# Kernel optimization log

Hardware: AMD Instinct MI355X
Metric: run time of the kernel (lower is better)

## Reference

```python
import jax, jax.numpy as jnp
import numpy as np

B, S, H, T = 32, 512, 1024, 32


def setup_inputs() -> dict:
    key = jax.random.key(0)
    ks = jax.random.split(key, 8)
    hidden = jax.random.normal(ks[0], (B, S, H), dtype=jnp.float32)
    W = jax.random.normal(ks[1], (H, T), dtype=jnp.float32) * 0.02
    b = jax.random.normal(ks[2], (T,), dtype=jnp.float32) * 0.02
    start_trans = jax.random.normal(ks[3], (T,), dtype=jnp.float32) * 0.1
    end_trans = jax.random.normal(ks[4], (T,), dtype=jnp.float32) * 0.1
    trans = jax.random.normal(ks[5], (T, T), dtype=jnp.float32) * 0.1
    tags = jax.random.randint(ks[6], (B, S), 0, T, dtype=jnp.int64)
    # variable-length mask: first position always valid (CRF requirement)
    lengths = jax.random.randint(ks[7], (B,), S // 2, S + 1)
    mask = jnp.arange(S)[None, :] < lengths[:, None]  # [B,S] bool
    return {"hidden": hidden, "W": W, "b": b, "start_trans": start_trans,
            "end_trans": end_trans, "trans": trans, "tags": tags, "mask": mask}


def reference(hidden, W, b, start_trans, end_trans, trans, tags, mask):
    # emission = log_softmax(fc(last_hidden_state))  [B,S,T]
    emissions = jax.nn.log_softmax(jnp.einsum('bsh,ht->bst', hidden, W) + b, axis=-1)
    maskf = mask.astype(emissions.dtype)

    # --- numerator: score of the gold tag path ---
    emit_tag = jnp.take_along_axis(emissions, tags[..., None], axis=-1)[..., 0]  # [B,S]
    trans_tag = trans[tags[:, :-1], tags[:, 1:]]                                  # [B,S-1]
    num = (start_trans[tags[:, 0]]
           + (emit_tag * maskf).sum(axis=1)
           + (trans_tag * maskf[:, 1:]).sum(axis=1))
    seq_len = mask.sum(axis=1).astype(jnp.int32)                                  # [B]
    last_tags = jnp.take_along_axis(tags, (seq_len - 1)[:, None].astype(tags.dtype), axis=1)[:, 0]
    num = num + end_trans[last_tags]

    # --- denominator: forward algorithm (masked logsumexp recurrence) ---
    alpha0 = start_trans[None, :] + emissions[:, 0]  # [B,T]

    def step(alpha, inp):
        em_t, m_t = inp  # [B,T], [B]
        nxt = jax.nn.logsumexp(alpha[:, :, None] + trans[None] + em_t[:, None, :], axis=1)
        return jnp.where(m_t[:, None], nxt, alpha), None

    em_rest = jnp.moveaxis(emissions[:, 1:], 1, 0)  # [S-1,B,T]
    m_rest = jnp.moveaxis(mask[:, 1:], 1, 0)        # [S-1,B]
    alpha, _ = jax.lax.scan(step, alpha0, (em_rest, m_rest))
    denom = jax.nn.logsumexp(alpha + end_trans[None], axis=1)  # [B]

    llh = num - denom        # CRF returns per-batch log-likelihood
    return -llh.mean()       # loss = (-crf(...)).mean()
```

## Files before the change

### kernel.cpp

```cpp
#include <hip/hip_runtime.h>
#include <hip/hip_bf16.h>


#define Bb 32
#define Ss 512
#define Hh 1024
#define Tt 32
#define NROWS (Bb*Ss)
#define NCHUNK 32
#define CHUNK_L 16

typedef __attribute__((ext_vector_type(8))) short bf16x8;
typedef __attribute__((ext_vector_type(4))) float f32x4;

__device__ __forceinline__ short f2bf(float f) {
  union { float f; unsigned u; } v; v.f = f;
  unsigned u = v.u;
  return (short)((u + 0x7FFFu + ((u >> 16) & 1u)) >> 16);
}

__global__ __launch_bounds__(128) void wpack_kernel(
    const float* __restrict__ W, short* __restrict__ Wpk,
    float* __restrict__ out) {
  const int k = blockIdx.x * 128 + threadIdx.x;
  if (k == 0) out[0] = 0.f;
#pragma unroll
  for (int t = 0; t < 32; ++t)
    Wpk[t * Hh + k] = f2bf(W[k * 32 + t]);
}

__global__ __launch_bounds__(256) void emis_fused_kernel(
    const float* __restrict__ hidden, const short* __restrict__ Wpk,
    const float* __restrict__ bias, float* __restrict__ logem) {
  __shared__ __align__(16) char smem[32768];
  float* red = (float*)smem;
  const int tid = threadIdx.x;
  const int wv = tid >> 6, lane = tid & 63;
  const int n = lane & 15, q = lane >> 4;
  const int row0 = blockIdx.x * 16;
  const int koff = wv * 256;

  {
    const int swv = tid >> 6;
    const int skc = (tid >> 3) & 7;
    const int sq = (tid >> 1) & 3;
    const int sj0 = (tid & 1) * 4;
    const int rbase = swv * 8192 + skc * 1024 + sj0 * 2;
    const int uxor = skc * 32;
    const float* hp = hidden + (size_t)row0 * Hh + 4 * tid;
#pragma unroll
    for (int i = 0; i < 16; ++i) {
      const float4 v = *(const float4*)(hp + (size_t)i * Hh);
      uint2 u;
      u.x = (unsigned short)f2bf(v.x) | ((unsigned)(unsigned short)f2bf(v.y) << 16);
      u.y = (unsigned short)f2bf(v.z) | ((unsigned)(unsigned short)f2bf(v.w) << 16);
      const int unit = ((i * 4 + sq) * 16) ^ uxor;
      *(uint2*)(smem + rbase + unit) = u;
    }
  }
  __syncthreads();

  const short* bpl = Wpk + n * Hh + koff;
  const short* bpr = Wpk + (16 + n) * Hh + koff;
  f32x4 d0 = {0.f, 0.f, 0.f, 0.f}, d1 = {0.f, 0.f, 0.f, 0.f};
#pragma unroll
  for (int kc = 0; kc < 8; ++kc) {
    const int aaddr = wv * 8192 + kc * 1024 + (((n * 4 + q) * 16) ^ (kc * 32));
    const bf16x8 a = *(const bf16x8*)(smem + aaddr);
    const bf16x8 wl = *(const bf16x8*)(bpl + kc * 32 + 8 * q);
    const bf16x8 wr = *(const bf16x8*)(bpr + kc * 32 + 8 * q);
    d0 = __builtin_amdgcn_mfma_f32_16x16x32_bf16(a, wl, d0, 0, 0, 0);
    d1 = __builtin_amdgcn_mfma_f32_16x16x32_bf16(a, wr, d1, 0, 0, 0);
  }
  __syncthreads();

#pragma unroll
  for (int r = 0; r < 4; ++r) {
    red[(wv * 16 + 4 * q + r) * 33 + n] = d0[r];
    red[(wv * 16 + 4 * q + r) * 33 + 16 + n] = d1[r];
  }
  __syncthreads();

  const int row = tid >> 4, c0 = tid & 15, c1 = 16 + c0;
  float v0 = 0.f, v1 = 0.f;
#pragma unroll
  for (int w = 0; w < 4; ++w) {
    v0 += red[(w * 16 + row) * 33 + c0];
    v1 += red[(w * 16 + row) * 33 + c1];
  }
  const float L0 = v0 + bias[c0], L1 = v1 + bias[c1];
  float mx = fmaxf(L0, L1);
#pragma unroll
  for (int d = 8; d >= 1; d >>= 1) mx = fmaxf(mx, __shfl_xor(mx, d, 16));
  float se = __expf(L0 - mx) + __expf(L1 - mx);
#pragma unroll
  for (int d = 8; d >= 1; d >>= 1) se += __shfl_xor(se, d, 16);
  const float corr = mx + __logf(se);
  const size_t rb = (size_t)(row0 + row) * Tt;
  logem[rb + c0] = L0 - corr;
  logem[rb + c1] = L1 - corr;
}

__global__ __launch_bounds__(256) void chunk_kernel(
    const float* __restrict__ logem, const float* __restrict__ trans,
    const int* __restrict__ mask, float* __restrict__ ecT,
    float* __restrict__ moff, float* __restrict__ cmax) {
  __shared__ __align__(16) float Pbuf[4 * 32 * 36];
  const int tid = threadIdx.x;
  const int wv = tid >> 6, lane = tid & 63;
  const int n = lane & 15, q = lane >> 4;
  const int chunk = blockIdx.x * 4 + wv;
  const int b = chunk >> 5, cc = chunk & 31;
  float* P = Pbuf + wv * 32 * 36;

  float etr0[8], etr1[8];
#pragma unroll
  for (int jj = 0; jj < 8; ++jj) {
    etr0[jj] = __expf(trans[(8 * q + jj) * 32 + n]);
    etr1[jj] = __expf(trans[(8 * q + jj) * 32 + 16 + n]);
  }

  const int t0 = 1 + cc * CHUNK_L;
  const int rowbase = b * Ss + t0;
  int pred = 0;
  if (lane < 16 && t0 + lane < Ss) pred = mask[rowbase + lane];
  const unsigned long long bal = __ballot(pred != 0);
  const int nst = __popcll(bal & 0xFFFFull);

  bf16x8 a0, a1;
#pragma unroll
  for (int jj = 0; jj < 8; ++jj) {
    a0[jj] = (n == 8 * q + jj) ? (short)0x3F80 : (short)0;
    a1[jj] = (16 + n == 8 * q + jj) ? (short)0x3F80 : (short)0;
  }

  f32x4 d00, d01, d10, d11;
  if (nst == 0) {
#pragma unroll
    for (int r = 0; r < 4; ++r) {
      d00[r] = (4 * q + r == n) ? 1.f : 0.f;
      d01[r] = 0.f;
      d10[r] = 0.f;
      d11[r] = (4 * q + r == n) ? 1.f : 0.f;
    }
  }
  float em0 = 0.f, em1 = 0.f;
  if (nst > 0) {
    em0 = __expf(logem[(size_t)rowbase * Tt + n]);
    em1 = __expf(logem[(size_t)rowbase * Tt + 16 + n]);
  }
  for (int st = 0; st < nst; ++st) {
    float em0n = 0.f, em1n = 0.f;
    if (st + 1 < nst) {
      em0n = __expf(logem[(size_t)(rowbase + st + 1) * Tt + n]);
      em1n = __expf(logem[(size_t)(rowbase + st + 1) * Tt + 16 + n]);
    }
    bf16x8 bL, bR;
#pragma unroll
    for (int jj = 0; jj < 8; ++jj) {
      bL[jj] = f2bf(etr0[jj] * em0);
      bR[jj] = f2bf(etr1[jj] * em1);
    }
    const f32x4 z = {0.f, 0.f, 0.f, 0.f};
    d00 = __builtin_amdgcn_mfma_f32_16x16x32_bf16(a0, bL, z, 0, 0, 0);
    d01 = __builtin_amdgcn_mfma_f32_16x16x32_bf16(a0, bR, z, 0, 0, 0);
    d10 = __builtin_amdgcn_mfma_f32_16x16x32_bf16(a1, bL, z, 0, 0, 0);
    d11 = __builtin_amdgcn_mfma_f32_16x16x32_bf16(a1, bR, z, 0, 0, 0);
    if (st + 1 < nst) {
#pragma unroll
      for (int r = 0; r < 4; ++r) {
        P[(4 * q + r) * 36 + n] = d00[r];
        P[(4 * q + r) * 36 + 16 + n] = d01[r];
        P[(16 + 4 * q + r) * 36 + n] = d10[r];
        P[(16 + 4 * q + r) * 36 + 16 + n] = d11[r];
      }
      asm volatile("s_waitcnt lgkmcnt(0)" ::: "memory");
      __builtin_amdgcn_sched_barrier(0);
      const float4 lo0 = *(const float4*)&P[n * 36 + 8 * q];
      const float4 lo1 = *(const float4*)&P[n * 36 + 8 * q + 4];
      const float4 hi0 = *(const float4*)&P[(16 + n) * 36 + 8 * q];
      const float4 hi1 = *(const float4*)&P[(16 + n) * 36 + 8 * q + 4];
      a0[0] = f2bf(lo0.x); a0[1] = f2bf(lo0.y); a0[2] = f2bf(lo0.z); a0[3] = f2bf(lo0.w);
      a0[4] = f2bf(lo1.x); a0[5] = f2bf(lo1.y); a0[6] = f2bf(lo1.z); a0[7] = f2bf(lo1.w);
      a1[0] = f2bf(hi0.x); a1[1] = f2bf(hi0.y); a1[2] = f2bf(hi0.z); a1[3] = f2bf(hi0.w);
      a1[4] = f2bf(hi1.x); a1[5] = f2bf(hi1.y); a1[6] = f2bf(hi1.z); a1[7] = f2bf(hi1.w);
    }
    em0 = em0n; em1 = em1n;
  }

  float lg0[4], lg1[4], iv0[4], iv1[4];
#pragma unroll
  for (int r = 0; r < 4; ++r) {
    float m0v = fmaxf(d00[r], d01[r]);
    float m1v = fmaxf(d10[r], d11[r]);
#pragma unroll
    for (int d = 8; d >= 1; d >>= 1) {
      m0v = fmaxf(m0v, __shfl_xor(m0v, d, 16));
      m1v = fmaxf(m1v, __shfl_xor(m1v, d, 16));
    }
    m0v = fmaxf(m0v, 1e-37f);
    m1v = fmaxf(m1v, 1e-37f);
    lg0[r] = __logf(m0v); iv0[r] = __builtin_amdgcn_rcpf(m0v);
    lg1[r] = __logf(m1v); iv1[r] = __builtin_amdgcn_rcpf(m1v);
  }
  float* E = ecT + (size_t)(b * NCHUNK + cc) * 32 * 32;
  {
    float4 s;
    s = make_float4(d00[0] * iv0[0], d00[1] * iv0[1], d00[2] * iv0[2], d00[3] * iv0[3]);
    *(float4*)&E[n * 32 + 4 * q] = s;
    s = make_float4(d10[0] * iv1[0], d10[1] * iv1[1], d10[2] * iv1[2], d10[3] * iv1[3]);
    *(float4*)&E[n * 32 + 16 + 4 * q] = s;
    s = make_float4(d01[0] * iv0[0], d01[1] * iv0[1], d01[2] * iv0[2], d01[3] * iv0[3]);
    *(float4*)&E[(16 + n) * 32 + 4 * q] = s;
    s = make_float4(d11[0] * iv1[0], d11[1] * iv1[1], d11[2] * iv1[2], d11[3] * iv1[3]);
    *(float4*)&E[(16 + n) * 32 + 16 + 4 * q] = s;
  }
  if (n == 0) {
    float* Mo = moff + (size_t)(b * NCHUNK + cc) * 32;
    *(float4*)&Mo[4 * q] = make_float4(lg0[0], lg0[1], lg0[2], lg0[3]);
    *(float4*)&Mo[16 + 4 * q] = make_float4(lg1[0], lg1[1], lg1[2], lg1[3]);
  }
  {
    float cm = fmaxf(fmaxf(fmaxf(lg0[0], lg0[1]), fmaxf(lg0[2], lg0[3])),
                     fmaxf(fmaxf(lg1[0], lg1[1]), fmaxf(lg1[2], lg1[3])));
    cm = fmaxf(cm, __shfl_xor(cm, 16));
    cm = fmaxf(cm, __shfl_xor(cm, 32));
    if (lane == 0) cmax[b * NCHUNK + cc] = cm;
  }
}

__global__ __launch_bounds__(64) void phase2_kernel(
    const float* __restrict__ logem, const float* __restrict__ start_trans,
    const float* __restrict__ end_trans, const float* __restrict__ ecT,
    const float* __restrict__ moff, const float* __restrict__ cmax,
    const float* __restrict__ trans, const int* __restrict__ tags,
    const int* __restrict__ mask, float* __restrict__ out) {
  const int b = blockIdx.x;
  const int lane = threadIdx.x;
  const int j = lane & 31;
  __shared__ __align__(16) float qlds[32];

  const int base_row = b * Ss;
  int lensum = 0;
  float snum = 0.f;
#pragma unroll
  for (int k = 0; k < 8; ++k) {
    const int ss = lane + 64 * k;
    const int m = mask[base_row + ss];
    lensum += m;
    if (m) {
      const int tg = tags[base_row + ss];
      snum += logem[(size_t)(base_row + ss) * Tt + tg];
      if (ss > 0) snum += trans[tags[base_row + ss - 1] * Tt + tg];
    }
  }
#pragma unroll
  for (int d = 32; d >= 1; d >>= 1) {
    snum += __shfl_xor(snum, d);
    lensum += __shfl_xor(lensum, d);
  }

  const float* base = ecT + (size_t)b * NCHUNK * 32 * 32;
  const float* mbase = moff + (size_t)b * NCHUNK * 32;
  const float cm_l = cmax[b * NCHUNK + j];

  float4 M[8], N[8];
  const float* r0 = base + j * 32;
#pragma unroll
  for (int k = 0; k < 8; ++k) M[k] = *(const float4*)(r0 + 4 * k);
  float mo_cur = mbase[j];

  float al0 = start_trans[j] + logem[(size_t)base_row * Tt + j];
  float m0 = al0;
#pragma unroll
  for (int d = 16; d >= 1; d >>= 1) m0 = fmaxf(m0, __shfl_xor(m0, d, 32));
  float a = __expf(al0 - m0);
  float Mb = m0;
  const float eend = __expf(end_trans[j]);

  float mo_next = 0.f;
  for (int c = 0; c < NCHUNK; ++c) {
    if (c + 1 < NCHUNK) {
      const float* rn = base + ((c + 1) * 32 + j) * 32;
#pragma unroll
      for (int k = 0; k < 8; ++k) N[k] = *(const float4*)(rn + 4 * k);
      mo_next = mbase[(c + 1) * 32 + j];
    }
    const float mom = __shfl(cm_l, c, 32);
    const float qv = a * __expf(mo_cur - mom);
    if (lane < 32) qlds[j] = qv;
    asm volatile("s_waitcnt lgkmcnt(0)" ::: "memory");
    __builtin_amdgcn_sched_barrier(0);
    float s0 = 0.f, s1 = 0.f, s2 = 0.f, s3 = 0.f;
#pragma unroll
    for (int k = 0; k < 8; ++k) {
      const float4 q4 = *(const float4*)(qlds + 4 * k);
      float* sp = (k & 1) ? ((k & 2) ? &s3 : &s1) : ((k & 2) ? &s2 : &s0);
      *sp = fmaf(q4.x, M[k].x, *sp);
      *sp = fmaf(q4.y, M[k].y, *sp);
      *sp = fmaf(q4.z, M[k].z, *sp);
      *sp = fmaf(q4.w, M[k].w, *sp);
    }
    const float s = (s0 + s1) + (s2 + s3);
    Mb += mom;
    if ((c & 3) == 3) {
      float m = s;
#pragma unroll
      for (int d = 16; d >= 1; d >>= 1) m = fmaxf(m, __shfl_xor(m, d, 32));
      m = fmaxf(m, 1e-30f);
      a = s * __builtin_amdgcn_rcpf(m);
      Mb += __logf(m);
    } else {
      a = s;
    }
#pragma unroll
    for (int k = 0; k < 8; ++k) M[k] = N[k];
    mo_cur = mo_next;
  }
  float z = a * eend;
#pragma unroll
  for (int d = 16; d >= 1; d >>= 1) z += __shfl_xor(z, d, 32);
  if (lane == 0) {
    const float numfull = snum + start_trans[tags[base_row]] +
                          end_trans[tags[base_row + lensum - 1]];
    const float denom = Mb + __logf(z);
    atomicAdd(out, -(numfull - denom) * (1.0f / 32.0f));
  }
}

extern "C" void kernel_launch(void* const* d_in, const int* in_sizes, int n_in,
                              void* d_out, int out_size, void* d_ws, size_t ws_size,
                              hipStream_t stream) {
  const float* hidden = (const float*)d_in[0];
  const float* W = (const float*)d_in[1];
  const float* bias = (const float*)d_in[2];
  const float* start_trans = (const float*)d_in[3];
  const float* end_trans = (const float*)d_in[4];
  const float* trans = (const float*)d_in[5];
  const int* tags = (const int*)d_in[6];
  const int* mask = (const int*)d_in[7];
  float* out = (float*)d_out;

  float* logem = (float*)d_ws;
  float* ecT = logem + (size_t)NROWS * Tt;
  float* moff = ecT + (size_t)Bb * NCHUNK * 32 * 32;
  float* cmax = moff + (size_t)Bb * NCHUNK * 32;
  short* Wpk = (short*)(cmax + (size_t)Bb * NCHUNK);

  wpack_kernel<<<8, 128, 0, stream>>>(W, Wpk, out);
  emis_fused_kernel<<<NROWS / 16, 256, 0, stream>>>(hidden, Wpk, bias, logem);
  chunk_kernel<<<Bb * NCHUNK / 4, 256, 0, stream>>>(logem, trans, mask, ecT, moff, cmax);
  phase2_kernel<<<Bb, 64, 0, stream>>>(logem, start_trans, end_trans, ecT, moff,
                                       cmax, trans, tags, mask, out);
}
```

Before: 151.1 us.

## Fuse chunk and phase2 kernels into one per-batch kernel with interleaved chunks

Merges the chunk-matrix kernel and the sequential phase2 kernel into a single per-batch block of 8 waves. Each wave processes two chunks interleaved per pass to hide MFMA and LDS latency. moff and cmax stay in shared memory, and the LDS ping-pong buffer is stored as bf16 so it reloads directly as MFMA operands. The emission factor is now applied after the MFMA instead of folded into the B operand. This removes one launch and some global traffic, but only 32 blocks run the chunk work, where the previous chunk kernel spread it over 256 blocks.

```diff
diff --git a/kernel.cpp b/kernel.cpp
--- a/kernel.cpp
+++ b/kernel.cpp
@@ -41,11 +41,10 @@
   const int koff = wv * 256;
 
   {
-    const int swv = tid >> 6;
     const int skc = (tid >> 3) & 7;
     const int sq = (tid >> 1) & 3;
     const int sj0 = (tid & 1) * 4;
-    const int rbase = swv * 8192 + skc * 1024 + sj0 * 2;
+    const int rbase = (tid >> 6) * 8192 + skc * 1024 + sj0 * 2;
     const int uxor = skc * 32;
     const float* hp = hidden + (size_t)row0 * Hh + 4 * tid;
 #pragma unroll
@@ -101,40 +100,10 @@
   logem[rb + c1] = L1 - corr;
 }
 
-__global__ __launch_bounds__(256) void chunk_kernel(
-    const float* __restrict__ logem, const float* __restrict__ trans,
-    const int* __restrict__ mask, float* __restrict__ ecT,
-    float* __restrict__ moff, float* __restrict__ cmax) {
-  __shared__ __align__(16) float Pbuf[4 * 32 * 36];
-  const int tid = threadIdx.x;
-  const int wv = tid >> 6, lane = tid & 63;
-  const int n = lane & 15, q = lane >> 4;
-  const int chunk = blockIdx.x * 4 + wv;
-  const int b = chunk >> 5, cc = chunk & 31;
-  float* P = Pbuf + wv * 32 * 36;
-
-  float etr0[8], etr1[8];
-#pragma unroll
-  for (int jj = 0; jj < 8; ++jj) {
-    etr0[jj] = __expf(trans[(8 * q + jj) * 32 + n]);
-    etr1[jj] = __expf(trans[(8 * q + jj) * 32 + 16 + n]);
-  }
-
-  const int t0 = 1 + cc * CHUNK_L;
-  const int rowbase = b * Ss + t0;
-  int pred = 0;
-  if (lane < 16 && t0 + lane < Ss) pred = mask[rowbase + lane];
-  const unsigned long long bal = __ballot(pred != 0);
-  const int nst = __popcll(bal & 0xFFFFull);
-
-  bf16x8 a0, a1;
-#pragma unroll
-  for (int jj = 0; jj < 8; ++jj) {
-    a0[jj] = (n == 8 * q + jj) ? (short)0x3F80 : (short)0;
-    a1[jj] = (16 + n == 8 * q + jj) ? (short)0x3F80 : (short)0;
-  }
-
-  f32x4 d00, d01, d10, d11;
+__device__ __forceinline__ void chunk_epilogue(
+    f32x4 d00, f32x4 d01, f32x4 d10, f32x4 d11, int nst,
+    int n, int q, int lane, float* __restrict__ E,
+    float* __restrict__ moff_row, float* __restrict__ cmaxp) {
   if (nst == 0) {
 #pragma unroll
     for (int r = 0; r < 4; ++r) {
@@ -144,50 +113,6 @@
       d11[r] = (4 * q + r == n) ? 1.f : 0.f;
     }
   }
-  float em0 = 0.f, em1 = 0.f;
-  if (nst > 0) {
-    em0 = __expf(logem[(size_t)rowbase * Tt + n]);
-    em1 = __expf(logem[(size_t)rowbase * Tt + 16 + n]);
-  }
-  for (int st = 0; st < nst; ++st) {
-    float em0n = 0.f, em1n = 0.f;
-    if (st + 1 < nst) {
-      em0n = __expf(logem[(size_t)(rowbase + st + 1) * Tt + n]);
-      em1n = __expf(logem[(size_t)(rowbase + st + 1) * Tt + 16 + n]);
-    }
-    bf16x8 bL, bR;
-#pragma unroll
-    for (int jj = 0; jj < 8; ++jj) {
-      bL[jj] = f2bf(etr0[jj] * em0);
-      bR[jj] = f2bf(etr1[jj] * em1);
-    }
-    const f32x4 z = {0.f, 0.f, 0.f, 0.f};
-    d00 = __builtin_amdgcn_mfma_f32_16x16x32_bf16(a0, bL, z, 0, 0, 0);
-    d01 = __builtin_amdgcn_mfma_f32_16x16x32_bf16(a0, bR, z, 0, 0, 0);
-    d10 = __builtin_amdgcn_mfma_f32_16x16x32_bf16(a1, bL, z, 0, 0, 0);
-    d11 = __builtin_amdgcn_mfma_f32_16x16x32_bf16(a1, bR, z, 0, 0, 0);
-    if (st + 1 < nst) {
-#pragma unroll
-      for (int r = 0; r < 4; ++r) {
-        P[(4 * q + r) * 36 + n] = d00[r];
-        P[(4 * q + r) * 36 + 16 + n] = d01[r];
-        P[(16 + 4 * q + r) * 36 + n] = d10[r];
-        P[(16 + 4 * q + r) * 36 + 16 + n] = d11[r];
-      }
-      asm volatile("s_waitcnt lgkmcnt(0)" ::: "memory");
-      __builtin_amdgcn_sched_barrier(0);
-      const float4 lo0 = *(const float4*)&P[n * 36 + 8 * q];
-      const float4 lo1 = *(const float4*)&P[n * 36 + 8 * q + 4];
-      const float4 hi0 = *(const float4*)&P[(16 + n) * 36 + 8 * q];
-      const float4 hi1 = *(const float4*)&P[(16 + n) * 36 + 8 * q + 4];
-      a0[0] = f2bf(lo0.x); a0[1] = f2bf(lo0.y); a0[2] = f2bf(lo0.z); a0[3] = f2bf(lo0.w);
-      a0[4] = f2bf(lo1.x); a0[5] = f2bf(lo1.y); a0[6] = f2bf(lo1.z); a0[7] = f2bf(lo1.w);
-      a1[0] = f2bf(hi0.x); a1[1] = f2bf(hi0.y); a1[2] = f2bf(hi0.z); a1[3] = f2bf(hi0.w);
-      a1[4] = f2bf(hi1.x); a1[5] = f2bf(hi1.y); a1[6] = f2bf(hi1.z); a1[7] = f2bf(hi1.w);
-    }
-    em0 = em0n; em1 = em1n;
-  }
-
   float lg0[4], lg1[4], iv0[4], iv1[4];
 #pragma unroll
   for (int r = 0; r < 4; ++r) {
@@ -203,7 +128,6 @@
     lg0[r] = __logf(m0v); iv0[r] = __builtin_amdgcn_rcpf(m0v);
     lg1[r] = __logf(m1v); iv1[r] = __builtin_amdgcn_rcpf(m1v);
   }
-  float* E = ecT + (size_t)(b * NCHUNK + cc) * 32 * 32;
   {
     float4 s;
     s = make_float4(d00[0] * iv0[0], d00[1] * iv0[1], d00[2] * iv0[2], d00[3] * iv0[3]);
@@ -216,59 +140,196 @@
     *(float4*)&E[(16 + n) * 32 + 16 + 4 * q] = s;
   }
   if (n == 0) {
-    float* Mo = moff + (size_t)(b * NCHUNK + cc) * 32;
-    *(float4*)&Mo[4 * q] = make_float4(lg0[0], lg0[1], lg0[2], lg0[3]);
-    *(float4*)&Mo[16 + 4 * q] = make_float4(lg1[0], lg1[1], lg1[2], lg1[3]);
-  }
+#pragma unroll
+    for (int r = 0; r < 4; ++r) {
+      moff_row[4 * q + r] = lg0[r];
+      moff_row[16 + 4 * q + r] = lg1[r];
+    }
+  }
+  float cm = fmaxf(fmaxf(fmaxf(lg0[0], lg0[1]), fmaxf(lg0[2], lg0[3])),
+                   fmaxf(fmaxf(lg1[0], lg1[1]), fmaxf(lg1[2], lg1[3])));
+  cm = fmaxf(cm, __shfl_xor(cm, 16));
+  cm = fmaxf(cm, __shfl_xor(cm, 32));
+  if (lane == 0) *cmaxp = cm;
+}
+
+__global__ __launch_bounds__(512) void batch_kernel(
+    const float* __restrict__ logem, const float* __restrict__ start_trans,
+    const float* __restrict__ end_trans, const float* __restrict__ trans,
+    const int* __restrict__ tags, const int* __restrict__ mask,
+    float* __restrict__ ecT, float* __restrict__ out) {
+  __shared__ __align__(16) short Pbuf[8][2][1280];
+  __shared__ __align__(16) float qlds[32];
+  __shared__ float moff_s[NCHUNK * 32];
+  __shared__ float cmax_s[NCHUNK];
+  __shared__ float numpart[8];
+  __shared__ int lenpart[8];
+
+  const int b = blockIdx.x;
+  const int tid = threadIdx.x;
+  const int wv = tid >> 6, lane = tid & 63;
+  const int n = lane & 15, q = lane >> 4;
+  const int base_row = b * Ss;
+
   {
-    float cm = fmaxf(fmaxf(fmaxf(lg0[0], lg0[1]), fmaxf(lg0[2], lg0[3])),
-                     fmaxf(fmaxf(lg1[0], lg1[1]), fmaxf(lg1[2], lg1[3])));
-    cm = fmaxf(cm, __shfl_xor(cm, 16));
-    cm = fmaxf(cm, __shfl_xor(cm, 32));
-    if (lane == 0) cmax[b * NCHUNK + cc] = cm;
-  }
-}
-
-__global__ __launch_bounds__(64) void phase2_kernel(
-    const float* __restrict__ logem, const float* __restrict__ start_trans,
-    const float* __restrict__ end_trans, const float* __restrict__ ecT,
-    const float* __restrict__ moff, const float* __restrict__ cmax,
-    const float* __restrict__ trans, const int* __restrict__ tags,
-    const int* __restrict__ mask, float* __restrict__ out) {
-  const int b = blockIdx.x;
-  const int lane = threadIdx.x;
+    float snum = 0.f;
+    int lensum = 0;
+    const int m = mask[base_row + tid];
+    lensum = m;
+    if (m) {
+      const int tg = tags[base_row + tid];
+      snum = logem[(size_t)(base_row + tid) * Tt + tg];
+      if (tid > 0) snum += trans[tags[base_row + tid - 1] * Tt + tg];
+    }
+#pragma unroll
+    for (int d = 32; d >= 1; d >>= 1) {
+      snum += __shfl_xor(snum, d);
+      lensum += __shfl_xor(lensum, d);
+    }
+    if (lane == 0) { numpart[wv] = snum; lenpart[wv] = lensum; }
+  }
+
+  bf16x8 bL, bR;
+#pragma unroll
+  for (int jj = 0; jj < 8; ++jj) {
+    bL[jj] = f2bf(__expf(trans[(8 * q + jj) * 32 + n]));
+    bR[jj] = f2bf(__expf(trans[(8 * q + jj) * 32 + 16 + n]));
+  }
+  const short idlo = (short)0, _unused = 0; (void)_unused; (void)idlo;
+
+  short* PA = &Pbuf[wv][0][0];
+  short* PB = &Pbuf[wv][1][0];
+
+  for (int pass = 0; pass < 2; ++pass) {
+    const int cA = 4 * wv + 2 * pass, cB = cA + 1;
+    const int t0A = 1 + cA * CHUNK_L, t0B = 1 + cB * CHUNK_L;
+    const int rowbaseA = base_row + t0A, rowbaseB = base_row + t0B;
+    int predA = 0, predB = 0;
+    if (lane < 16) {
+      if (t0A + lane < Ss) predA = mask[rowbaseA + lane];
+      if (t0B + lane < Ss) predB = mask[rowbaseB + lane];
+    }
+    const int nstA = __popcll(__ballot(predA != 0) & 0xFFFFull);
+    const int nstB = __popcll(__ballot(predB != 0) & 0xFFFFull);
+
+    bf16x8 aA0, aA1, aB0, aB1;
+#pragma unroll
+    for (int jj = 0; jj < 8; ++jj) {
+      const short ilo = (n == 8 * q + jj) ? (short)0x3F80 : (short)0;
+      const short ihi = (16 + n == 8 * q + jj) ? (short)0x3F80 : (short)0;
+      aA0[jj] = ilo; aA1[jj] = ihi;
+      aB0[jj] = ilo; aB1[jj] = ihi;
+    }
+
+    f32x4 dA00 = {0,0,0,0}, dA01 = {0,0,0,0}, dA10 = {0,0,0,0}, dA11 = {0,0,0,0};
+    f32x4 dB00 = {0,0,0,0}, dB01 = {0,0,0,0}, dB10 = {0,0,0,0}, dB11 = {0,0,0,0};
+
+    float emA0 = 0.f, emA1 = 0.f, emB0 = 0.f, emB1 = 0.f;
+    if (nstA > 0) {
+      emA0 = __expf(logem[(size_t)rowbaseA * Tt + n]);
+      emA1 = __expf(logem[(size_t)rowbaseA * Tt + 16 + n]);
+    }
+    if (nstB > 0) {
+      emB0 = __expf(logem[(size_t)rowbaseB * Tt + n]);
+      emB1 = __expf(logem[(size_t)rowbaseB * Tt + 16 + n]);
+    }
+
+    const int nmax = nstA > nstB ? nstA : nstB;
+    for (int st = 0; st < nmax; ++st) {
+      float emA0n = 0.f, emA1n = 0.f, emB0n = 0.f, emB1n = 0.f;
+      if (st + 1 < nstA) {
+        emA0n = __expf(logem[(size_t)(rowbaseA + st + 1) * Tt + n]);
+        emA1n = __expf(logem[(size_t)(rowbaseA + st + 1) * Tt + 16 + n]);
+      }
+      if (st + 1 < nstB) {
+        emB0n = __expf(logem[(size_t)(rowbaseB + st + 1) * Tt + n]);
+        emB1n = __expf(logem[(size_t)(rowbaseB + st + 1) * Tt + 16 + n]);
+      }
+      const f32x4 z = {0.f, 0.f, 0.f, 0.f};
+      if (st < nstA) {
+        dA00 = __builtin_amdgcn_mfma_f32_16x16x32_bf16(aA0, bL, z, 0, 0, 0);
+        dA01 = __builtin_amdgcn_mfma_f32_16x16x32_bf16(aA0, bR, z, 0, 0, 0);
+        dA10 = __builtin_amdgcn_mfma_f32_16x16x32_bf16(aA1, bL, z, 0, 0, 0);
+        dA11 = __builtin_amdgcn_mfma_f32_16x16x32_bf16(aA1, bR, z, 0, 0, 0);
+#pragma unroll
+        for (int r = 0; r < 4; ++r) {
+          dA00[r] *= emA0; dA01[r] *= emA1;
+          dA10[r] *= emA0; dA11[r] *= emA1;
+        }
+      }
+      if (st < nstB) {
+        dB00 = __builtin_amdgcn_mfma_f32_16x16x32_bf16(aB0, bL, z, 0, 0, 0);
+        dB01 = __builtin_amdgcn_mfma_f32_16x16x32_bf16(aB0, bR, z, 0, 0, 0);
+        dB10 = __builtin_amdgcn_mfma_f32_16x16x32_bf16(aB1, bL, z, 0, 0, 0);
+        dB11 = __builtin_amdgcn_mfma_f32_16x16x32_bf16(aB1, bR, z, 0, 0, 0);
+#pragma unroll
+        for (int r = 0; r < 4; ++r) {
+          dB00[r] *= emB0; dB01[r] *= emB1;
+          dB10[r] *= emB0; dB11[r] *= emB1;
+        }
+      }
+      const bool wA = (st + 1 < nstA), wB = (st + 1 < nstB);
+      if (wA) {
+#pragma unroll
+        for (int r = 0; r < 4; ++r) {
+          PA[(4 * q + r) * 40 + n] = f2bf(dA00[r]);
+          PA[(4 * q + r) * 40 + 16 + n] = f2bf(dA01[r]);
+          PA[(16 + 4 * q + r) * 40 + n] = f2bf(dA10[r]);
+          PA[(16 + 4 * q + r) * 40 + 16 + n] = f2bf(dA11[r]);
+        }
+      }
+      if (wB) {
+#pragma unroll
+        for (int r = 0; r < 4; ++r) {
+          PB[(4 * q + r) * 40 + n] = f2bf(dB00[r]);
+          PB[(4 * q + r) * 40 + 16 + n] = f2bf(dB01[r]);
+          PB[(16 + 4 * q + r) * 40 + n] = f2bf(dB10[r]);
+          PB[(16 + 4 * q + r) * 40 + 16 + n] = f2bf(dB11[r]);
+        }
+      }
+      if (wA | wB) {
+        asm volatile("s_waitcnt lgkmcnt(0)" ::: "memory");
+        __builtin_amdgcn_sched_barrier(0);
+      }
+      if (wA) {
+        aA0 = *(const bf16x8*)(PA + n * 40 + 8 * q);
+        aA1 = *(const bf16x8*)(PA + (16 + n) * 40 + 8 * q);
+      }
+      if (wB) {
+        aB0 = *(const bf16x8*)(PB + n * 40 + 8 * q);
+        aB1 = *(const bf16x8*)(PB + (16 + n) * 40 + 8 * q);
+      }
+      emA0 = emA0n; emA1 = emA1n; emB0 = emB0n; emB1 = emB1n;
+    }
+
+    chunk_epilogue(dA00, dA01, dA10, dA11, nstA, n, q, lane,
+                   ecT + (size_t)(b * NCHUNK + cA) * 32 * 32,
+                   moff_s + cA * 32, cmax_s + cA);
+    chunk_epilogue(dB00, dB01, dB10, dB11, nstB, n, q, lane,
+                   ecT + (size_t)(b * NCHUNK + cB) * 32 * 32,
+                   moff_s + cB * 32, cmax_s + cB);
+  }
+
+  __syncthreads();
+  if (wv != 0) return;
+
   const int j = lane & 31;
-  __shared__ __align__(16) float qlds[32];
-
-  const int base_row = b * Ss;
-  int lensum = 0;
-  float snum = 0.f;
-#pragma unroll
-  for (int k = 0; k < 8; ++k) {
-    const int ss = lane + 64 * k;
-    const int m = mask[base_row + ss];
-    lensum += m;
-    if (m) {
-      const int tg = tags[base_row + ss];
-      snum += logem[(size_t)(base_row + ss) * Tt + tg];
-      if (ss > 0) snum += trans[tags[base_row + ss - 1] * Tt + tg];
-    }
-  }
+  float sn = (lane < 8) ? numpart[lane] : 0.f;
+  int ln = (lane < 8) ? lenpart[lane] : 0;
 #pragma unroll
   for (int d = 32; d >= 1; d >>= 1) {
-    snum += __shfl_xor(snum, d);
-    lensum += __shfl_xor(lensum, d);
+    sn += __shfl_xor(sn, d);
+    ln += __shfl_xor(ln, d);
   }
 
   const float* base = ecT + (size_t)b * NCHUNK * 32 * 32;
-  const float* mbase = moff + (size_t)b * NCHUNK * 32;
-  const float cm_l = cmax[b * NCHUNK + j];
+  const float cm_l = cmax_s[j];
 
   float4 M[8], N[8];
   const float* r0 = base + j * 32;
 #pragma unroll
   for (int k = 0; k < 8; ++k) M[k] = *(const float4*)(r0 + 4 * k);
-  float mo_cur = mbase[j];
+  float mo_cur = moff_s[j];
 
   float al0 = start_trans[j] + logem[(size_t)base_row * Tt + j];
   float m0 = al0;
@@ -284,7 +345,7 @@
       const float* rn = base + ((c + 1) * 32 + j) * 32;
 #pragma unroll
       for (int k = 0; k < 8; ++k) N[k] = *(const float4*)(rn + 4 * k);
-      mo_next = mbase[(c + 1) * 32 + j];
+      mo_next = moff_s[(c + 1) * 32 + j];
     }
     const float mom = __shfl(cm_l, c, 32);
     const float qv = a * __expf(mo_cur - mom);
@@ -321,8 +382,8 @@
 #pragma unroll
   for (int d = 16; d >= 1; d >>= 1) z += __shfl_xor(z, d, 32);
   if (lane == 0) {
-    const float numfull = snum + start_trans[tags[base_row]] +
-                          end_trans[tags[base_row + lensum - 1]];
+    const float numfull = sn + start_trans[tags[base_row]] +
+                          end_trans[tags[base_row + ln - 1]];
     const float denom = Mb + __logf(z);
     atomicAdd(out, -(numfull - denom) * (1.0f / 32.0f));
   }
@@ -343,13 +404,10 @@
 
   float* logem = (float*)d_ws;
   float* ecT = logem + (size_t)NROWS * Tt;
-  float* moff = ecT + (size_t)Bb * NCHUNK * 32 * 32;
-  float* cmax = moff + (size_t)Bb * NCHUNK * 32;
-  short* Wpk = (short*)(cmax + (size_t)Bb * NCHUNK);
+  short* Wpk = (short*)(ecT + (size_t)Bb * NCHUNK * 32 * 32);
 
   wpack_kernel<<<8, 128, 0, stream>>>(W, Wpk, out);
   emis_fused_kernel<<<NROWS / 16, 256, 0, stream>>>(hidden, Wpk, bias, logem);
-  chunk_kernel<<<Bb * NCHUNK / 4, 256, 0, stream>>>(logem, trans, mask, ecT, moff, cmax);
-  phase2_kernel<<<Bb, 64, 0, stream>>>(logem, start_trans, end_trans, ecT, moff,
-                                       cmax, trans, tags, mask, out);
-}
+  batch_kernel<<<Bb, 512, 0, stream>>>(logem, start_trans, end_trans, trans,
+                                       tags, mask, ecT, out);
+}
```

Measured after the change: 165.4 us. 1.09x slower.

## Combine four chunk transfer matrices per block via MFMA tree reduction

Applied to the files above, without the earlier changes.

Each block now multiplies its four 16-step chunk transfer matrices together in shared memory, using a two-level MFMA tree with per-row log-scale renormalization. It writes one super-chunk matrix per block instead of four. The sequential phase2 scan then runs 8 iterations per batch instead of 32, which shortens the serial critical path and cuts ecT traffic. The cost is extra bf16 rounding in the matrix products, which may reduce accuracy, plus two block-wide syncs in the chunk kernel.

```diff
diff --git a/kernel.cpp b/kernel.cpp
--- a/kernel.cpp
+++ b/kernel.cpp
@@ -9,6 +9,7 @@
 #define NROWS (Bb*Ss)
 #define NCHUNK 32
 #define CHUNK_L 16
+#define NSUP 8
 
 typedef __attribute__((ext_vector_type(8))) short bf16x8;
 typedef __attribute__((ext_vector_type(4))) float f32x4;
@@ -17,6 +18,11 @@
   union { float f; unsigned u; } v; v.f = f;
   unsigned u = v.u;
   return (short)((u + 0x7FFFu + ((u >> 16) & 1u)) >> 16);
+}
+__device__ __forceinline__ float bf2f(short s) {
+  union { unsigned u; float f; } v;
+  v.u = ((unsigned)(unsigned short)s) << 16;
+  return v.f;
 }
 
 __global__ __launch_bounds__(128) void wpack_kernel(
@@ -41,11 +47,10 @@
   const int koff = wv * 256;
 
   {
-    const int swv = tid >> 6;
     const int skc = (tid >> 3) & 7;
     const int sq = (tid >> 1) & 3;
     const int sj0 = (tid & 1) * 4;
-    const int rbase = swv * 8192 + skc * 1024 + sj0 * 2;
+    const int rbase = (tid >> 6) * 8192 + skc * 1024 + sj0 * 2;
     const int uxor = skc * 32;
     const float* hp = hidden + (size_t)row0 * Hh + 4 * tid;
 #pragma unroll
@@ -101,17 +106,59 @@
   logem[rb + c1] = L1 - corr;
 }
 
+__device__ __forceinline__ void combine32(
+    const short* __restrict__ Ea, const short* __restrict__ Eb,
+    const float* __restrict__ Oa, const float* __restrict__ Ob, float obmax,
+    int n, int q,
+    f32x4& c00, f32x4& c01, f32x4& c10, f32x4& c11,
+    float* __restrict__ lgn0, float* __restrict__ lgn1,
+    float* __restrict__ iv0, float* __restrict__ iv1) {
+  const bf16x8 a0 = *(const bf16x8*)(Ea + n * 40 + 8 * q);
+  const bf16x8 a1 = *(const bf16x8*)(Ea + (16 + n) * 40 + 8 * q);
+  bf16x8 bL, bR;
+#pragma unroll
+  for (int jj = 0; jj < 8; ++jj) {
+    const float sc = __expf(Ob[8 * q + jj] - obmax);
+    bL[jj] = f2bf(bf2f(Eb[(8 * q + jj) * 40 + n]) * sc);
+    bR[jj] = f2bf(bf2f(Eb[(8 * q + jj) * 40 + 16 + n]) * sc);
+  }
+  const f32x4 z = {0.f, 0.f, 0.f, 0.f};
+  c00 = __builtin_amdgcn_mfma_f32_16x16x32_bf16(a0, bL, z, 0, 0, 0);
+  c01 = __builtin_amdgcn_mfma_f32_16x16x32_bf16(a0, bR, z, 0, 0, 0);
+  c10 = __builtin_amdgcn_mfma_f32_16x16x32_bf16(a1, bL, z, 0, 0, 0);
+  c11 = __builtin_amdgcn_mfma_f32_16x16x32_bf16(a1, bR, z, 0, 0, 0);
+#pragma unroll
+  for (int r = 0; r < 4; ++r) {
+    float m0v = fmaxf(c00[r], c01[r]);
+    float m1v = fmaxf(c10[r], c11[r]);
+#pragma unroll
+    for (int d = 8; d >= 1; d >>= 1) {
+      m0v = fmaxf(m0v, __shfl_xor(m0v, d, 16));
+      m1v = fmaxf(m1v, __shfl_xor(m1v, d, 16));
+    }
+    m0v = fmaxf(m0v, 1e-37f);
+    m1v = fmaxf(m1v, 1e-37f);
+    iv0[r] = __builtin_amdgcn_rcpf(m0v);
+    iv1[r] = __builtin_amdgcn_rcpf(m1v);
+    lgn0[r] = Oa[4 * q + r] + obmax + __logf(m0v);
+    lgn1[r] = Oa[16 + 4 * q + r] + obmax + __logf(m1v);
+  }
+}
+
 __global__ __launch_bounds__(256) void chunk_kernel(
     const float* __restrict__ logem, const float* __restrict__ trans,
-    const int* __restrict__ mask, float* __restrict__ ecT,
-    float* __restrict__ moff, float* __restrict__ cmax) {
-  __shared__ __align__(16) float Pbuf[4 * 32 * 36];
+    const int* __restrict__ mask, float* __restrict__ ecT4,
+    float* __restrict__ moff4, float* __restrict__ cmax4) {
+  __shared__ __align__(16) float Pbuf[4][32 * 36];
+  __shared__ __align__(16) short Ebuf[4][32][40];
+  __shared__ float Obuf[4][32];
+  __shared__ float Cmx[4];
   const int tid = threadIdx.x;
   const int wv = tid >> 6, lane = tid & 63;
   const int n = lane & 15, q = lane >> 4;
   const int chunk = blockIdx.x * 4 + wv;
   const int b = chunk >> 5, cc = chunk & 31;
-  float* P = Pbuf + wv * 32 * 36;
+  float* P = &Pbuf[wv][0];
 
   float etr0[8], etr1[8];
 #pragma unroll
@@ -188,51 +235,107 @@
     em0 = em0n; em1 = em1n;
   }
 
-  float lg0[4], lg1[4], iv0[4], iv1[4];
-#pragma unroll
-  for (int r = 0; r < 4; ++r) {
-    float m0v = fmaxf(d00[r], d01[r]);
-    float m1v = fmaxf(d10[r], d11[r]);
-#pragma unroll
-    for (int d = 8; d >= 1; d >>= 1) {
-      m0v = fmaxf(m0v, __shfl_xor(m0v, d, 16));
-      m1v = fmaxf(m1v, __shfl_xor(m1v, d, 16));
-    }
-    m0v = fmaxf(m0v, 1e-37f);
-    m1v = fmaxf(m1v, 1e-37f);
-    lg0[r] = __logf(m0v); iv0[r] = __builtin_amdgcn_rcpf(m0v);
-    lg1[r] = __logf(m1v); iv1[r] = __builtin_amdgcn_rcpf(m1v);
-  }
-  float* E = ecT + (size_t)(b * NCHUNK + cc) * 32 * 32;
   {
-    float4 s;
-    s = make_float4(d00[0] * iv0[0], d00[1] * iv0[1], d00[2] * iv0[2], d00[3] * iv0[3]);
-    *(float4*)&E[n * 32 + 4 * q] = s;
-    s = make_float4(d10[0] * iv1[0], d10[1] * iv1[1], d10[2] * iv1[2], d10[3] * iv1[3]);
-    *(float4*)&E[n * 32 + 16 + 4 * q] = s;
-    s = make_float4(d01[0] * iv0[0], d01[1] * iv0[1], d01[2] * iv0[2], d01[3] * iv0[3]);
-    *(float4*)&E[(16 + n) * 32 + 4 * q] = s;
-    s = make_float4(d11[0] * iv1[0], d11[1] * iv1[1], d11[2] * iv1[2], d11[3] * iv1[3]);
-    *(float4*)&E[(16 + n) * 32 + 16 + 4 * q] = s;
-  }
-  if (n == 0) {
-    float* Mo = moff + (size_t)(b * NCHUNK + cc) * 32;
-    *(float4*)&Mo[4 * q] = make_float4(lg0[0], lg0[1], lg0[2], lg0[3]);
-    *(float4*)&Mo[16 + 4 * q] = make_float4(lg1[0], lg1[1], lg1[2], lg1[3]);
-  }
-  {
+    float lg0[4], lg1[4], iv0[4], iv1[4];
+#pragma unroll
+    for (int r = 0; r < 4; ++r) {
+      float m0v = fmaxf(d00[r], d01[r]);
+      float m1v = fmaxf(d10[r], d11[r]);
+#pragma unroll
+      for (int d = 8; d >= 1; d >>= 1) {
+        m0v = fmaxf(m0v, __shfl_xor(m0v, d, 16));
+        m1v = fmaxf(m1v, __shfl_xor(m1v, d, 16));
+      }
+      m0v = fmaxf(m0v, 1e-37f);
+      m1v = fmaxf(m1v, 1e-37f);
+      lg0[r] = __logf(m0v); iv0[r] = __builtin_amdgcn_rcpf(m0v);
+      lg1[r] = __logf(m1v); iv1[r] = __builtin_amdgcn_rcpf(m1v);
+    }
+#pragma unroll
+    for (int r = 0; r < 4; ++r) {
+      Ebuf[wv][4 * q + r][n] = f2bf(d00[r] * iv0[r]);
+      Ebuf[wv][4 * q + r][16 + n] = f2bf(d01[r] * iv0[r]);
+      Ebuf[wv][16 + 4 * q + r][n] = f2bf(d10[r] * iv1[r]);
+      Ebuf[wv][16 + 4 * q + r][16 + n] = f2bf(d11[r] * iv1[r]);
+    }
+    if (n == 0) {
+#pragma unroll
+      for (int r = 0; r < 4; ++r) {
+        Obuf[wv][4 * q + r] = lg0[r];
+        Obuf[wv][16 + 4 * q + r] = lg1[r];
+      }
+    }
     float cm = fmaxf(fmaxf(fmaxf(lg0[0], lg0[1]), fmaxf(lg0[2], lg0[3])),
                      fmaxf(fmaxf(lg1[0], lg1[1]), fmaxf(lg1[2], lg1[3])));
     cm = fmaxf(cm, __shfl_xor(cm, 16));
     cm = fmaxf(cm, __shfl_xor(cm, 32));
-    if (lane == 0) cmax[b * NCHUNK + cc] = cm;
+    if (lane == 0) Cmx[wv] = cm;
+  }
+  __syncthreads();
+
+  if (wv < 2) {
+    const int ai = 2 * wv, bi = 2 * wv + 1;
+    f32x4 c00, c01, c10, c11;
+    float lg0[4], lg1[4], iv0[4], iv1[4];
+    combine32(&Ebuf[ai][0][0], &Ebuf[bi][0][0], Obuf[ai], Obuf[bi], Cmx[bi],
+              n, q, c00, c01, c10, c11, lg0, lg1, iv0, iv1);
+#pragma unroll
+    for (int r = 0; r < 4; ++r) {
+      Ebuf[ai][4 * q + r][n] = f2bf(c00[r] * iv0[r]);
+      Ebuf[ai][4 * q + r][16 + n] = f2bf(c01[r] * iv0[r]);
+      Ebuf[ai][16 + 4 * q + r][n] = f2bf(c10[r] * iv1[r]);
+      Ebuf[ai][16 + 4 * q + r][16 + n] = f2bf(c11[r] * iv1[r]);
+    }
+    if (n == 0) {
+#pragma unroll
+      for (int r = 0; r < 4; ++r) {
+        Obuf[ai][4 * q + r] = lg0[r];
+        Obuf[ai][16 + 4 * q + r] = lg1[r];
+      }
+    }
+    float cm = fmaxf(fmaxf(fmaxf(lg0[0], lg0[1]), fmaxf(lg0[2], lg0[3])),
+                     fmaxf(fmaxf(lg1[0], lg1[1]), fmaxf(lg1[2], lg1[3])));
+    cm = fmaxf(cm, __shfl_xor(cm, 16));
+    cm = fmaxf(cm, __shfl_xor(cm, 32));
+    if (lane == 0) Cmx[ai] = cm;
+  }
+  __syncthreads();
+
+  if (wv == 0) {
+    f32x4 c00, c01, c10, c11;
+    float lg0[4], lg1[4], iv0[4], iv1[4];
+    combine32(&Ebuf[0][0][0], &Ebuf[2][0][0], Obuf[0], Obuf[2], Cmx[2],
+              n, q, c00, c01, c10, c11, lg0, lg1, iv0, iv1);
+    const int sup = blockIdx.x;
+    float* E = ecT4 + (size_t)sup * 32 * 32;
+    {
+      float4 s;
+      s = make_float4(c00[0] * iv0[0], c00[1] * iv0[1], c00[2] * iv0[2], c00[3] * iv0[3]);
+      *(float4*)&E[n * 32 + 4 * q] = s;
+      s = make_float4(c10[0] * iv1[0], c10[1] * iv1[1], c10[2] * iv1[2], c10[3] * iv1[3]);
+      *(float4*)&E[n * 32 + 16 + 4 * q] = s;
+      s = make_float4(c01[0] * iv0[0], c01[1] * iv0[1], c01[2] * iv0[2], c01[3] * iv0[3]);
+      *(float4*)&E[(16 + n) * 32 + 4 * q] = s;
+      s = make_float4(c11[0] * iv1[0], c11[1] * iv1[1], c11[2] * iv1[2], c11[3] * iv1[3]);
+      *(float4*)&E[(16 + n) * 32 + 16 + 4 * q] = s;
+    }
+    if (n == 0) {
+      float* Mo = moff4 + (size_t)sup * 32;
+      *(float4*)&Mo[4 * q] = make_float4(lg0[0], lg0[1], lg0[2], lg0[3]);
+      *(float4*)&Mo[16 + 4 * q] = make_float4(lg1[0], lg1[1], lg1[2], lg1[3]);
+    }
+    float cm = fmaxf(fmaxf(fmaxf(lg0[0], lg0[1]), fmaxf(lg0[2], lg0[3])),
+                     fmaxf(fmaxf(lg1[0], lg1[1]), fmaxf(lg1[2], lg1[3])));
+    cm = fmaxf(cm, __shfl_xor(cm, 16));
+    cm = fmaxf(cm, __shfl_xor(cm, 32));
+    if (lane == 0) cmax4[sup] = cm;
   }
 }
 
 __global__ __launch_bounds__(64) void phase2_kernel(
     const float* __restrict__ logem, const float* __restrict__ start_trans,
-    const float* __restrict__ end_trans, const float* __restrict__ ecT,
-    const float* __restrict__ moff, const float* __restrict__ cmax,
+    const float* __restrict__ end_trans, const float* __restrict__ ecT4,
+    const float* __restrict__ moff4, const float* __restrict__ cmax4,
     const float* __restrict__ trans, const int* __restrict__ tags,
     const int* __restrict__ mask, float* __restrict__ out) {
   const int b = blockIdx.x;
@@ -260,9 +363,9 @@
     lensum += __shfl_xor(lensum, d);
   }
 
-  const float* base = ecT + (size_t)b * NCHUNK * 32 * 32;
-  const float* mbase = moff + (size_t)b * NCHUNK * 32;
-  const float cm_l = cmax[b * NCHUNK + j];
+  const float* base = ecT4 + (size_t)b * NSUP * 32 * 32;
+  const float* mbase = moff4 + (size_t)b * NSUP * 32;
+  const float cm_l = (j < NSUP) ? cmax4[b * NSUP + j] : 0.f;
 
   float4 M[8], N[8];
   const float* r0 = base + j * 32;
@@ -279,8 +382,8 @@
   const float eend = __expf(end_trans[j]);
 
   float mo_next = 0.f;
-  for (int c = 0; c < NCHUNK; ++c) {
-    if (c + 1 < NCHUNK) {
+  for (int c = 0; c < NSUP; ++c) {
+    if (c + 1 < NSUP) {
       const float* rn = base + ((c + 1) * 32 + j) * 32;
 #pragma unroll
       for (int k = 0; k < 8; ++k) N[k] = *(const float4*)(rn + 4 * k);
@@ -342,14 +445,15 @@
   float* out = (float*)d_out;
 
   float* logem = (float*)d_ws;
-  float* ecT = logem + (size_t)NROWS * Tt;
-  float* moff = ecT + (size_t)Bb * NCHUNK * 32 * 32;
-  float* cmax = moff + (size_t)Bb * NCHUNK * 32;
-  short* Wpk = (short*)(cmax + (size_t)Bb * NCHUNK);
+  float* ecT4 = logem + (size_t)NROWS * Tt;
+  float* moff4 = ecT4 + (size_t)Bb * NSUP * 32 * 32;
+  float* cmax4 = moff4 + (size_t)Bb * NSUP * 32;
+  short* Wpk = (short*)(cmax4 + (size_t)Bb * NSUP);
 
   wpack_kernel<<<8, 128, 0, stream>>>(W, Wpk, out);
   emis_fused_kernel<<<NROWS / 16, 256, 0, stream>>>(hidden, Wpk, bias, logem);
-  chunk_kernel<<<Bb * NCHUNK / 4, 256, 0, stream>>>(logem, trans, mask, ecT, moff, cmax);
-  phase2_kernel<<<Bb, 64, 0, stream>>>(logem, start_trans, end_trans, ecT, moff,
-                                       cmax, trans, tags, mask, out);
-}
+  chunk_kernel<<<Bb * NCHUNK / 4, 256, 0, stream>>>(logem, trans, mask,
+                                                    ecT4, moff4, cmax4);
+  phase2_kernel<<<Bb, 64, 0, stream>>>(logem, start_trans, end_trans, ecT4,
+                                       moff4, cmax4, trans, tags, mask, out);
+}
```

Measured after the change: 140.8 us, median of 2. -6.8%, faster.
